# Kernel optimization log

Measured on AMD Instinct MI355X. Metric: run time of the kernel, lower is better.

The kernel has to match this reference:

```python
import jax, jax.numpy as jnp
import numpy as np

COMMITMENT_COST = 0.25
CODE_BOOK_SIZE = 1024
EMBED_DIM = 64


def setup_inputs() -> dict:
    key = jax.random.key(0)
    k1, k2 = jax.random.split(key)
    inputs = jax.random.normal(k1, (32, 64, 32, 32), dtype=jnp.float32)
    # matches torch init: uniform(-1/K, 1/K)
    embedding = jax.random.uniform(
        k2, (CODE_BOOK_SIZE, EMBED_DIM), dtype=jnp.float32,
        minval=-1.0 / CODE_BOOK_SIZE, maxval=1.0 / CODE_BOOK_SIZE)
    return {"inputs": inputs, "embedding": embedding}


def reference(inputs, embedding):
    # inputs: [B, D, H, W] -> [B, H, W, D]
    x = jnp.transpose(inputs, (0, 2, 3, 1))
    B, H, W, D = x.shape
    flat = x.reshape(-1, D)                                   # [N, D]
    # ((x - e)**2).mean(-1), without the [N, K, D] broadcast tensor)
    x2 = jnp.sum(flat * flat, axis=1, keepdims=True)          # [N, 1]
    e2 = jnp.sum(embedding * embedding, axis=1)               # [K]
    distances = (x2 - 2.0 * (flat @ embedding.T) + e2) / D    # [N, K]
    encoding_indices = jnp.argmin(distances, axis=1)          # [N]
    quantized = embedding[encoding_indices].reshape(B, H, W, D)
    e_latent_loss = jnp.mean((jax.lax.stop_gradient(quantized) - x) ** 2)
    q_latent_loss = jnp.mean((quantized - jax.lax.stop_gradient(x)) ** 2)
    loss = q_latent_loss + COMMITMENT_COST * e_latent_loss
    # straight-through estimator (training mode); value identical to quantized
    quantized = x + jax.lax.stop_gradient(quantized - x)
    return (loss,
            jnp.transpose(quantized, (0, 3, 1, 2)),
            encoding_indices.reshape(B, -1))
```

## Files before the change

kernel.cpp:

```cpp
#include <hip/hip_runtime.h>


constexpr int D_   = 64;
constexpr int HW   = 1024;
constexpr int K_   = 1024;
constexpr int PTS  = 128;
constexpr int CK   = 512;
constexpr int DH   = 32;
constexpr int SP   = 132;
constexpr int QE   = 2097152;
constexpr int IDX_OFF = 1 + QE;

__global__ __launch_bounds__(1024, 4) void vq_main_kernel(
    const float* __restrict__ in, const float* __restrict__ emb,
    float* __restrict__ out, float* __restrict__ loss_acc,
    unsigned* __restrict__ cnt) {
  __shared__ float eTs[DH * CK];
  __shared__ float xT[D_ * SP];
  __shared__ float e2s[K_];
  __shared__ float x2s[PTS];
  __shared__ int   idx_sel[PTS];
  __shared__ float redbuf[8];

  const int t    = threadIdx.x;
  const int lane = t & 63;
  const int wv   = t >> 6;
  const int p0   = wv * 8;
  const int blk  = blockIdx.x;
  const int b    = blk >> 3;
  const int hw0  = (blk & 7) * PTS;
  const float* inb = in + b * (D_ * HW) + hw0;

  const int kl = t & 511;
  const int h  = t >> 9;
  const int pos = ((kl >> 2) & 1) * 256 + (kl >> 3) * 4 + (kl & 3);

#pragma unroll
  for (int i = 0; i < 2; ++i) {
    int fi = t + i * 1024;
    int d  = fi >> 5, p4 = fi & 31;
    *(float4*)(&xT[d * SP + p4 * 4]) = *(const float4*)(inb + d * HW + p4 * 4);
  }

  {
    const float4* e4 = (const float4*)(emb + t * 64);
    float s = 0.f;
#pragma unroll
    for (int q = 0; q < 16; ++q) {
      float4 v = e4[q];
      s += v.x * v.x; s += v.y * v.y; s += v.z * v.z; s += v.w * v.w;
    }
    e2s[t] = s;
  }

  {
    const float4* g = (const float4*)(emb + kl * 64 + h * 16);
    float4 v0 = g[0], v1 = g[1], v2 = g[2], v3 = g[3];
    int dq = h * 16;
    eTs[(dq + 0) * CK + pos] = v0.x; eTs[(dq + 1) * CK + pos] = v0.y;
    eTs[(dq + 2) * CK + pos] = v0.z; eTs[(dq + 3) * CK + pos] = v0.w;
    eTs[(dq + 4) * CK + pos] = v1.x; eTs[(dq + 5) * CK + pos] = v1.y;
    eTs[(dq + 6) * CK + pos] = v1.z; eTs[(dq + 7) * CK + pos] = v1.w;
    eTs[(dq + 8) * CK + pos] = v2.x; eTs[(dq + 9) * CK + pos] = v2.y;
    eTs[(dq +10) * CK + pos] = v2.z; eTs[(dq +11) * CK + pos] = v2.w;
    eTs[(dq +12) * CK + pos] = v3.x; eTs[(dq +13) * CK + pos] = v3.y;
    eTs[(dq +14) * CK + pos] = v3.z; eTs[(dq +15) * CK + pos] = v3.w;
  }
  __syncthreads();

  if (t < PTS) {
    float s = 0.f;
#pragma unroll 8
    for (int d = 0; d < D_; ++d) { float xv = xT[d * SP + t]; s = fmaf(xv, xv, s); }
    x2s[t] = s;
  }
  __syncthreads();

  float minv[8]; int mini[8];
#pragma unroll
  for (int i = 0; i < 8; ++i) { minv[i] = 3.4e38f; mini[i] = 0; }

#pragma unroll 1
  for (int c = 0; c < 2; ++c) {
    float acc[8][8];
#pragma unroll
    for (int i = 0; i < 8; ++i)
#pragma unroll
      for (int j = 0; j < 8; ++j) acc[i][j] = 0.f;

#pragma unroll 1
    for (int dh = 0; dh < 2; ++dh) {
      const int s = c * 2 + dh;

      const float* ep = &eTs[lane * 4];
      const float* xp = &xT[dh * DH * SP + p0];
#pragma unroll 2
      for (int dd = 0; dd < DH; ++dd) {
        float4 e0 = *(const float4*)(ep);
        float4 e1 = *(const float4*)(ep + 256);
        float4 xa = *(const float4*)(xp);
        float4 xb = *(const float4*)(xp + 4);
        ep += CK; xp += SP;
        float xf[8] = {xa.x, xa.y, xa.z, xa.w, xb.x, xb.y, xb.z, xb.w};
        float ef[8] = {e0.x, e0.y, e0.z, e0.w, e1.x, e1.y, e1.z, e1.w};
#pragma unroll
        for (int i = 0; i < 8; ++i)
#pragma unroll
          for (int j = 0; j < 8; ++j)
            acc[i][j] = fmaf(xf[i], ef[j], acc[i][j]);
      }

      if (s < 3) {
        __syncthreads();
        const int cn = (s + 1) >> 1, dn = (s + 1) & 1;
        const float4* g =
            (const float4*)(emb + (cn * CK + kl) * 64 + dn * DH + h * 16);
        float4 v0 = g[0], v1 = g[1], v2 = g[2], v3 = g[3];
        int dq = h * 16;
        eTs[(dq + 0) * CK + pos] = v0.x; eTs[(dq + 1) * CK + pos] = v0.y;
        eTs[(dq + 2) * CK + pos] = v0.z; eTs[(dq + 3) * CK + pos] = v0.w;
        eTs[(dq + 4) * CK + pos] = v1.x; eTs[(dq + 5) * CK + pos] = v1.y;
        eTs[(dq + 6) * CK + pos] = v1.z; eTs[(dq + 7) * CK + pos] = v1.w;
        eTs[(dq + 8) * CK + pos] = v2.x; eTs[(dq + 9) * CK + pos] = v2.y;
        eTs[(dq +10) * CK + pos] = v2.z; eTs[(dq +11) * CK + pos] = v2.w;
        eTs[(dq +12) * CK + pos] = v3.x; eTs[(dq +13) * CK + pos] = v3.y;
        eTs[(dq +14) * CK + pos] = v3.z; eTs[(dq +15) * CK + pos] = v3.w;
        __syncthreads();
      }
    }

    float x2v[8];
    {
      float4 xa = *(const float4*)&x2s[p0];
      float4 xb = *(const float4*)&x2s[p0 + 4];
      x2v[0]=xa.x; x2v[1]=xa.y; x2v[2]=xa.z; x2v[3]=xa.w;
      x2v[4]=xb.x; x2v[5]=xb.y; x2v[6]=xb.z; x2v[7]=xb.w;
    }
    float e2f[8];
    {
      const float4* p4 = (const float4*)&e2s[c * CK + lane * 8];
      float4 v0 = p4[0], v1 = p4[1];
      e2f[0]=v0.x; e2f[1]=v0.y; e2f[2]=v0.z; e2f[3]=v0.w;
      e2f[4]=v1.x; e2f[5]=v1.y; e2f[6]=v1.z; e2f[7]=v1.w;
    }
#pragma unroll
    for (int j = 0; j < 8; ++j) {
      int cg = c * CK + lane * 8 + j;
      float e2v = e2f[j];
#pragma unroll
      for (int i = 0; i < 8; ++i) {
        float u = fmaf(-2.f, acc[i][j], x2v[i]) + e2v;
        if (u < minv[i]) { minv[i] = u; mini[i] = cg; }
      }
    }
  }

#pragma unroll
  for (int i = 0; i < 8; ++i) {
    float v = minv[i]; int ix = mini[i];
#pragma unroll
    for (int off = 1; off < 64; off <<= 1) {
      float vo = __shfl_xor(v, off);
      int   io = __shfl_xor(ix, off);
      if (vo < v || (vo == v && io < ix)) { v = vo; ix = io; }
    }
    if (lane == 0) idx_sel[p0 + i] = ix;
  }
  __syncthreads();

  if (t < PTS) out[IDX_OFF + blk * PTS + t] = (float)idx_sel[t];

  float* outq = out + 1 + b * (D_ * HW) + hw0;
  float lp = 0.f;
  if (t < 512) {
#pragma unroll
    for (int i = 0; i < 4; ++i) {
      int fi = t + i * 512;
      int p = fi & 127, qd = fi >> 7;
      int cidx = idx_sel[p];
      float4 q = *(const float4*)(emb + cidx * 64 + qd * 4);
      float xv0 = xT[(qd * 4 + 0) * SP + p];
      float xv1 = xT[(qd * 4 + 1) * SP + p];
      float xv2 = xT[(qd * 4 + 2) * SP + p];
      float xv3 = xT[(qd * 4 + 3) * SP + p];
      float d0 = q.x - xv0, d1 = q.y - xv1, d2 = q.z - xv2, d3 = q.w - xv3;
      lp = fmaf(d0, d0, lp); lp = fmaf(d1, d1, lp);
      lp = fmaf(d2, d2, lp); lp = fmaf(d3, d3, lp);
      outq[(qd * 4 + 0) * HW + p] = xv0 + d0;
      outq[(qd * 4 + 1) * HW + p] = xv1 + d1;
      outq[(qd * 4 + 2) * HW + p] = xv2 + d2;
      outq[(qd * 4 + 3) * HW + p] = xv3 + d3;
    }

#pragma unroll
    for (int off = 1; off < 64; off <<= 1) lp += __shfl_xor(lp, off);
    if ((t & 63) == 0) redbuf[t >> 6] = lp;
  }
  __syncthreads();
  if (t == 0) {
    float part = 0.f;
#pragma unroll
    for (int w = 0; w < 8; ++w) part += redbuf[w];
    atomicAdd(loss_acc, part);
    __threadfence();
    unsigned old = atomicAdd(cnt, 1u);
    if (old == 255u) {
      __threadfence();
      float total = atomicAdd(loss_acc, 0.0f);
      float m = total * (1.0f / 2097152.0f);
      out[0] = m + 0.25f * m;
    }
  }
}

extern "C" void kernel_launch(void* const* d_in, const int* in_sizes, int n_in,
                              void* d_out, int out_size, void* d_ws, size_t ws_size,
                              hipStream_t stream) {
  const float* in  = (const float*)d_in[0];
  const float* emb = (const float*)d_in[1];
  float* out = (float*)d_out;
  float* loss_acc = (float*)d_ws;
  unsigned* cnt   = (unsigned*)d_ws + 4;

  hipMemsetAsync(d_ws, 0, 64, stream);
  vq_main_kernel<<<256, 1024, 0, stream>>>(in, emb, out, loss_acc, cnt);
}
```

Baseline: 138.1 us.

## Load input points via scalar s_load into SGPRs instead of LDS reads

The inner distance loop now reads each wave's 8 point values straight from global memory with inline-asm s_load_dwordx8 into scalar registers, and no longer reads the transposed xT tile from LDS. The 32-step loop is fully unrolled into 8 groups of 4 d-rows, which cuts LDS traffic to codebook reads only and lets the FMAs take SGPR operands. In exchange, each group waits on a full lgkmcnt(0), serialising scalar memory latency with the LDS codebook loads. SGPR pressure and code size also grow.

```diff
diff --git a/kernel.cpp b/kernel.cpp
--- a/kernel.cpp
+++ b/kernel.cpp
@@ -10,6 +10,57 @@
 constexpr int SP   = 132;
 constexpr int QE   = 2097152;
 constexpr int IDX_OFF = 1 + QE;
+
+typedef int v8i __attribute__((ext_vector_type(8)));
+
+template <int BYTEOFF>
+__device__ __forceinline__ void xload4(unsigned long long base,
+                                       v8i& q0, v8i& q1, v8i& q2, v8i& q3) {
+  asm volatile(
+      "s_waitcnt lgkmcnt(0)\n\t"
+      "s_load_dwordx8 %0, %4, %5\n\t"
+      "s_load_dwordx8 %1, %4, %6\n\t"
+      "s_load_dwordx8 %2, %4, %7\n\t"
+      "s_load_dwordx8 %3, %4, %8\n\t"
+      "s_waitcnt lgkmcnt(0)"
+      : "=&s"(q0), "=&s"(q1), "=&s"(q2), "=&s"(q3)
+      : "s"(base), "n"(BYTEOFF), "n"(BYTEOFF + 4096), "n"(BYTEOFF + 8192),
+        "n"(BYTEOFF + 12288));
+}
+
+#define DD1(QV)                                                        \
+  {                                                                    \
+    float4 e0 = *(const float4*)(ep);           \
+    float4 e1 = *(const float4*)(ep + 256);     \
+    ep += CK;                                                          \
+    float ef[8] = {e0.x, e0.y, e0.z, e0.w, e1.x, e1.y, e1.z, e1.w};    \
+    _Pragma("unroll") for (int i = 0; i < 8; ++i) {                    \
+      float xsv = __int_as_float((QV)[i]);                             \
+      _Pragma("unroll") for (int j = 0; j < 8; ++j)                    \
+          acc[i][j] = fmaf(xsv, ef[j], acc[i][j]);                     \
+    }                                                                  \
+  }
+
+#define GRP(OFF)                                                       \
+  {                                                                    \
+    v8i qa, qb, qc, qd;                                                \
+    xload4<OFF>(xbase, qa, qb, qc, qd);                                \
+    DD1(qa) DD1(qb) DD1(qc) DD1(qd)                                    \
+  }
+
+template <int DHI>
+__device__ __forceinline__ void stage32(float (&acc)[8][8], const float* eTs,
+                                        int lane, unsigned long long xbase) {
+  const float* ep = eTs + lane * 4;
+  GRP(DHI * 131072 + 0 * 16384)
+  GRP(DHI * 131072 + 1 * 16384)
+  GRP(DHI * 131072 + 2 * 16384)
+  GRP(DHI * 131072 + 3 * 16384)
+  GRP(DHI * 131072 + 4 * 16384)
+  GRP(DHI * 131072 + 5 * 16384)
+  GRP(DHI * 131072 + 6 * 16384)
+  GRP(DHI * 131072 + 7 * 16384)
+}
 
 __global__ __launch_bounds__(1024, 4) void vq_main_kernel(
     const float* __restrict__ in, const float* __restrict__ emb,
@@ -34,6 +85,11 @@
   const int kl = t & 511;
   const int h  = t >> 9;
   const int pos = ((kl >> 2) & 1) * 256 + (kl >> 3) * 4 + (kl & 3);
+
+  unsigned long long xaddr = (unsigned long long)(const void*)(inb + p0);
+  unsigned xlo = __builtin_amdgcn_readfirstlane((unsigned)xaddr);
+  unsigned xhi = __builtin_amdgcn_readfirstlane((unsigned)(xaddr >> 32));
+  const unsigned long long xbase = ((unsigned long long)xhi << 32) | xlo;
 
 #pragma unroll
   for (int i = 0; i < 2; ++i) {
@@ -88,28 +144,9 @@
 #pragma unroll
       for (int j = 0; j < 8; ++j) acc[i][j] = 0.f;
 
-#pragma unroll 1
-    for (int dh = 0; dh < 2; ++dh) {
-      const int s = c * 2 + dh;
-
-      const float* ep = &eTs[lane * 4];
-      const float* xp = &xT[dh * DH * SP + p0];
-#pragma unroll 2
-      for (int dd = 0; dd < DH; ++dd) {
-        float4 e0 = *(const float4*)(ep);
-        float4 e1 = *(const float4*)(ep + 256);
-        float4 xa = *(const float4*)(xp);
-        float4 xb = *(const float4*)(xp + 4);
-        ep += CK; xp += SP;
-        float xf[8] = {xa.x, xa.y, xa.z, xa.w, xb.x, xb.y, xb.z, xb.w};
-        float ef[8] = {e0.x, e0.y, e0.z, e0.w, e1.x, e1.y, e1.z, e1.w};
-#pragma unroll
-        for (int i = 0; i < 8; ++i)
-#pragma unroll
-          for (int j = 0; j < 8; ++j)
-            acc[i][j] = fmaf(xf[i], ef[j], acc[i][j]);
-      }
-
+    stage32<0>(acc, eTs, lane, xbase);
+    {
+      const int s = c * 2;
       if (s < 3) {
         __syncthreads();
         const int cn = (s + 1) >> 1, dn = (s + 1) & 1;
@@ -129,12 +166,34 @@
       }
     }
 
+    stage32<1>(acc, eTs, lane, xbase);
+    {
+      const int s = c * 2 + 1;
+      if (s < 3) {
+        __syncthreads();
+        const int cn = (s + 1) >> 1, dn = (s + 1) & 1;
+        const float4* g =
+            (const float4*)(emb + (cn * CK + kl) * 64 + dn * DH + h * 16);
+        float4 v0 = g[0], v1 = g[1], v2 = g[2], v3 = g[3];
+        int dq = h * 16;
+        eTs[(dq + 0) * CK + pos] = v0.x; eTs[(dq + 1) * CK + pos] = v0.y;
+        eTs[(dq + 2) * CK + pos] = v0.z; eTs[(dq + 3) * CK + pos] = v0.w;
+        eTs[(dq + 4) * CK + pos] = v1.x; eTs[(dq + 5) * CK + pos] = v1.y;
+        eTs[(dq + 6) * CK + pos] = v1.z; eTs[(dq + 7) * CK + pos] = v1.w;
+        eTs[(dq + 8) * CK + pos] = v2.x; eTs[(dq + 9) * CK + pos] = v2.y;
+        eTs[(dq +10) * CK + pos] = v2.z; eTs[(dq +11) * CK + pos] = v2.w;
+        eTs[(dq +12) * CK + pos] = v3.x; eTs[(dq +13) * CK + pos] = v3.y;
+        eTs[(dq +14) * CK + pos] = v3.z; eTs[(dq +15) * CK + pos] = v3.w;
+        __syncthreads();
+      }
+    }
+
     float x2v[8];
     {
-      float4 xa = *(const float4*)&x2s[p0];
-      float4 xb = *(const float4*)&x2s[p0 + 4];
-      x2v[0]=xa.x; x2v[1]=xa.y; x2v[2]=xa.z; x2v[3]=xa.w;
-      x2v[4]=xb.x; x2v[5]=xb.y; x2v[6]=xb.z; x2v[7]=xb.w;
+      float4 xa2 = *(const float4*)&x2s[p0];
+      float4 xb2 = *(const float4*)&x2s[p0 + 4];
+      x2v[0]=xa2.x; x2v[1]=xa2.y; x2v[2]=xa2.z; x2v[3]=xa2.w;
+      x2v[4]=xb2.x; x2v[5]=xb2.y; x2v[6]=xb2.z; x2v[7]=xb2.w;
     }
     float e2f[8];
     {
```

New measurement: 541.3 us. +291.8%, slower.
